# Kernel tuning notes

Hardware: AMD Instinct MI355X
Metric: run time of the kernel (lower is better)

Reference implementation:

```python
import jax, jax.numpy as jnp
import numpy as np

D_MODEL, N_HEADS, D_FF = 768, 12, 3072
B, S = 2, 2048
EPS = 1e-6

def _ln(x, alpha, bias):
    # Matches torch: std with Bessel correction (unbiased), scalar alpha/bias
    mean = x.mean(axis=-1, keepdims=True)
    std = jnp.std(x, axis=-1, keepdims=True, ddof=1)
    return alpha * (x - mean) / (std + EPS) + bias

def setup_inputs() -> dict:
    key = jax.random.key(0)
    ks = jax.random.split(key, 12)
    def w(k, shp):
        return jax.random.normal(k, shp, dtype=jnp.float32) * 0.02
    inp = {
        "x": jax.random.normal(ks[0], (B, S, D_MODEL), dtype=jnp.float32),
        "mask": jnp.ones((B, 1, 1, S), dtype=jnp.int32),
        "wq": w(ks[1], (D_MODEL, D_MODEL)), "bq": jnp.zeros((D_MODEL,), jnp.float32),
        "wk": w(ks[2], (D_MODEL, D_MODEL)), "bk": jnp.zeros((D_MODEL,), jnp.float32),
        "wv": w(ks[3], (D_MODEL, D_MODEL)), "bv": jnp.zeros((D_MODEL,), jnp.float32),
        "wo": w(ks[4], (D_MODEL, D_MODEL)), "bo": jnp.zeros((D_MODEL,), jnp.float32),
        "w1": w(ks[5], (D_MODEL, D_FF)), "b1": jnp.zeros((D_FF,), jnp.float32),
        "w2": w(ks[6], (D_FF, D_MODEL)), "b2": jnp.zeros((D_MODEL,), jnp.float32),
        "ln1_a": jnp.ones((1,), jnp.float32), "ln1_b": jnp.zeros((1,), jnp.float32),
        "ln2_a": jnp.ones((1,), jnp.float32), "ln2_b": jnp.zeros((1,), jnp.float32),
    }
    return inp

def reference(x, mask, wq, bq, wk, bk, wv, bv, wo, bo, w1, b1, w2, b2,
              ln1_a, ln1_b, ln2_a, ln2_b):
    d_k = D_MODEL // N_HEADS
    # --- residual 1: pre-LN self-attention ---
    h = _ln(x, ln1_a, ln1_b)
    q = (h @ wq + bq).reshape(B, S, N_HEADS, d_k).transpose(0, 2, 1, 3)
    k = (h @ wk + bk).reshape(B, S, N_HEADS, d_k).transpose(0, 2, 1, 3)
    v = (h @ wv + bv).reshape(B, S, N_HEADS, d_k).transpose(0, 2, 1, 3)
    scores = jnp.einsum('bhqd,bhkd->bhqk', q, k) / jnp.sqrt(jnp.float32(d_k))
    scores = jnp.where(mask == 0, jnp.float32(-1e9), scores)
    attn = jax.nn.softmax(scores, axis=-1)            # [B,H,S,S] materialized, as in source
    ctx = jnp.einsum('bhqk,bhkd->bhqd', attn, v)
    ctx = ctx.transpose(0, 2, 1, 3).reshape(B, S, D_MODEL)
    x = x + (ctx @ wo + bo)
    # --- residual 2: pre-LN FFN ---
    h = _ln(x, ln2_a, ln2_b)
    ffn = jax.nn.relu(h @ w1 + b1) @ w2 + b2
    return x + ffn
```

## Files before the change

### kernel.cpp

```cpp
#include <hip/hip_runtime.h>
#include <math.h>

#define DM    768
#define NH    12
#define DKH   64
#define DFF   3072
#define BATCH 2
#define SLEN  2048
#define MTOT  4096
#define LNEPS 1e-6f
#define QSCALE 0.18033688011112042f

typedef unsigned short u16;
typedef __attribute__((ext_vector_type(8))) short bf16x8;
typedef __attribute__((ext_vector_type(4))) float f32x4;
typedef __attribute__((ext_vector_type(4))) unsigned short us4;

__device__ __forceinline__ u16 f2bf(float f) {
    union { float f; unsigned int u; } v; v.f = f;
    unsigned int r = v.u + 0x7FFFu + ((v.u >> 16) & 1u);
    return (u16)(r >> 16);
}

__device__ __forceinline__ unsigned pk2bf(float lo, float hi) {
    union { float f; unsigned u; } a, b;
    a.f = lo; b.f = hi;
    return __builtin_amdgcn_perm(b.u + 0x8000u, a.u + 0x8000u, 0x07060302u);
}

__device__ __forceinline__ void gld16(const void* g, void* lds) {
    __builtin_amdgcn_global_load_lds(
        (const __attribute__((address_space(1))) unsigned int*)(unsigned long long)g,
        (__attribute__((address_space(3))) unsigned int*)(unsigned int)(unsigned long long)lds,
        16, 0, 0);
}

__global__ __launch_bounds__(256) void ln_kernel(const float* __restrict__ x,
                                                 u16* __restrict__ out,
                                                 const float* __restrict__ alpha_p,
                                                 const float* __restrict__ beta_p) {
    int row = blockIdx.x;
    const float* xr = x + (size_t)row * DM;
    int t = threadIdx.x;
    float v0 = xr[t], v1 = xr[t + 256], v2 = xr[t + 512];
    float s = v0 + v1 + v2;
    #pragma unroll
    for (int off = 32; off > 0; off >>= 1) s += __shfl_down(s, off);
    __shared__ float red[4], red2[4];
    int wv = t >> 6, ln = t & 63;
    if (ln == 0) red[wv] = s;
    __syncthreads();
    float mean = (red[0] + red[1] + red[2] + red[3]) * (1.0f / 768.0f);
    float d0 = v0 - mean, d1 = v1 - mean, d2 = v2 - mean;
    float sq = d0 * d0 + d1 * d1 + d2 * d2;
    #pragma unroll
    for (int off = 32; off > 0; off >>= 1) sq += __shfl_down(sq, off);
    if (ln == 0) red2[wv] = sq;
    __syncthreads();
    float var = (red2[0] + red2[1] + red2[2] + red2[3]) * (1.0f / 767.0f);
    float scale = alpha_p[0] / (sqrtf(var) + LNEPS);
    float bias = beta_p[0];
    u16* orow = out + (size_t)row * DM;
    orow[t]       = f2bf(d0 * scale + bias);
    orow[t + 256] = f2bf(d1 * scale + bias);
    orow[t + 512] = f2bf(d2 * scale + bias);
}

__global__ __launch_bounds__(256) void wcast_all(
        const float* __restrict__ wq, const float* __restrict__ wk,
        const float* __restrict__ wv, const float* __restrict__ wo,
        const float* __restrict__ w1, const float* __restrict__ w2,
        u16* __restrict__ wqT, u16* __restrict__ wkT, u16* __restrict__ wvT,
        u16* __restrict__ woT, u16* __restrict__ w1T, u16* __restrict__ w2T) {
    __shared__ float tile[32][33];
    int bid = blockIdx.x;
    const float* src; u16* dst; int R, C, bx, by;
    if (bid < 2304) {
        int j = bid / 576, tix = bid % 576;
        R = 768; C = 768; bx = tix % 24; by = tix / 24;
        src = (j == 0) ? wq : (j == 1) ? wk : (j == 2) ? wv : wo;
        dst = (j == 0) ? wqT : (j == 1) ? wkT : (j == 2) ? wvT : woT;
    } else if (bid < 4608) {
        int tix = bid - 2304;
        R = 768; C = 3072; bx = tix % 96; by = tix / 96;
        src = w1; dst = w1T;
    } else {
        int tix = bid - 4608;
        R = 3072; C = 768; bx = tix % 24; by = tix / 24;
        src = w2; dst = w2T;
    }
    int t = threadIdx.x, tx = t & 31, ty = t >> 5;
    int r0 = by * 32, c0 = bx * 32;
    #pragma unroll
    for (int p = 0; p < 4; p++)
        tile[ty + p * 8][tx] = src[(size_t)(r0 + ty + p * 8) * C + c0 + tx];
    __syncthreads();
    #pragma unroll
    for (int p = 0; p < 4; p++)
        dst[(size_t)(c0 + ty + p * 8) * R + r0 + tx] = f2bf(tile[tx][ty + p * 8]);
}

template<int EPI>
__device__ __forceinline__ void gemm128_core(const u16* __restrict__ A,
                                             const u16* __restrict__ Wt,
                                             const float* __restrict__ bias,
                                             const float* __restrict__ resid,
                                             void* __restrict__ Cout,
                                             int M, int N, int Kstride, int Kloop,
                                             float scale, int bm, int bn) {
    __shared__ __align__(16) u16 As[2][128 * 32];
    __shared__ __align__(16) u16 Bs[2][128 * 32];
    int t = threadIdx.x;
    int ln = t & 63, w = t >> 6;
    int wm = w >> 1, wn = w & 1;
    int quad = ln >> 4, col = ln & 15;
    int m0 = bm * 128, n0 = bn * 128;

    f32x4 acc[4][4];
    const f32x4 zero = {0.f, 0.f, 0.f, 0.f};
    #pragma unroll
    for (int i = 0; i < 4; i++)
        #pragma unroll
        for (int j = 0; j < 4; j++) acc[i][j] = zero;

    const u16* Ag = A  + (size_t)(m0 + 32 * w + (ln >> 2)) * Kstride + (ln & 3) * 8;
    const u16* Bg = Wt + (size_t)(n0 + 32 * w + (ln >> 2)) * Kstride + (ln & 3) * 8;

    gld16(Ag,                As[0] + w * 1024);
    gld16(Ag + 16 * Kstride, As[0] + w * 1024 + 512);
    gld16(Bg,                Bs[0] + w * 1024);
    gld16(Bg + 16 * Kstride, Bs[0] + w * 1024 + 512);
    __syncthreads();

    for (int k0 = 0; k0 < Kloop; k0 += 32) {
        int cur = (k0 >> 5) & 1, nxt = cur ^ 1;
        if (k0 + 32 < Kloop) {
            gld16(Ag + k0 + 32,                As[nxt] + w * 1024);
            gld16(Ag + k0 + 32 + 16 * Kstride, As[nxt] + w * 1024 + 512);
            gld16(Bg + k0 + 32,                Bs[nxt] + w * 1024);
            gld16(Bg + k0 + 32 + 16 * Kstride, Bs[nxt] + w * 1024 + 512);
        }
        bf16x8 af[4], bfr[4];
        #pragma unroll
        for (int i = 0; i < 4; i++)
            af[i] = *(const bf16x8*)&As[cur][(wm * 64 + i * 16 + col) * 32 + quad * 8];
        #pragma unroll
        for (int j = 0; j < 4; j++)
            bfr[j] = *(const bf16x8*)&Bs[cur][(wn * 64 + j * 16 + col) * 32 + quad * 8];
        #pragma unroll
        for (int i = 0; i < 4; i++)
            #pragma unroll
            for (int j = 0; j < 4; j++)
                acc[i][j] = __builtin_amdgcn_mfma_f32_16x16x32_bf16(af[i], bfr[j], acc[i][j], 0, 0, 0);
        __syncthreads();
    }

    #pragma unroll
    for (int i = 0; i < 4; i++) {
        int mb = m0 + wm * 64 + i * 16 + quad * 4;
        #pragma unroll
        for (int j = 0; j < 4; j++) {
            int n = n0 + wn * 64 + j * 16 + col;
            if (EPI == 0 || EPI == 1) {
                float bs = bias[n];
                u16* Cb = (u16*)Cout;
                #pragma unroll
                for (int r = 0; r < 4; r++) {
                    float f = (acc[i][j][r] + bs) * ((EPI == 0) ? scale : 1.0f);
                    if (EPI == 1) f = fmaxf(f, 0.f);
                    Cb[(size_t)(mb + r) * N + n] = f2bf(f);
                }
            } else if (EPI == 2) {
                float bs = bias[n];
                float* Cf = (float*)Cout;
                #pragma unroll
                for (int r = 0; r < 4; r++)
                    Cf[(size_t)(mb + r) * N + n] =
                        acc[i][j][r] + bs + resid[(size_t)(mb + r) * N + n];
            } else if (EPI == 3) {
                float bs = bias[n];
                u16* Cb = (u16*)Cout;
                us4 pk;
                #pragma unroll
                for (int r = 0; r < 4; r++) pk[r] = f2bf(acc[i][j][r] + bs);
                *(us4*)&Cb[(size_t)n * M + mb] = pk;
            } else {
                float* Cf = (float*)Cout;
                #pragma unroll
                for (int r = 0; r < 4; r++)
                    atomicAdd(&Cf[(size_t)(mb + r) * N + n], acc[i][j][r]);
            }
        }
    }
}

template<int EPI>
__global__ __launch_bounds__(256) void gemm_kernel(const u16* __restrict__ A,
                                                   const u16* __restrict__ Wt,
                                                   const float* __restrict__ bias,
                                                   const float* __restrict__ resid,
                                                   void* __restrict__ C,
                                                   int M, int N, int Kstride, int Kloop,
                                                   float scale) {
    const u16* Az = A  + (size_t)blockIdx.z * Kloop;
    const u16* Wz = Wt + (size_t)blockIdx.z * Kloop;
    gemm128_core<EPI>(Az, Wz, bias, resid, C, M, N, Kstride, Kloop, scale,
                      blockIdx.y, blockIdx.x);
}

__global__ __launch_bounds__(256) void qkv_kernel(const u16* __restrict__ h,
        const u16* __restrict__ wqT, const u16* __restrict__ wkT, const u16* __restrict__ wvT,
        const float* __restrict__ bq, const float* __restrict__ bk, const float* __restrict__ bv,
        u16* __restrict__ q, u16* __restrict__ k, u16* __restrict__ vT) {
    int z = blockIdx.z;
    if (z == 0)      gemm128_core<0>(h, wqT, bq, nullptr, q,  MTOT, DM, DM, DM, QSCALE, blockIdx.y, blockIdx.x);
    else if (z == 1) gemm128_core<0>(h, wkT, bk, nullptr, k,  MTOT, DM, DM, DM, 1.0f,   blockIdx.y, blockIdx.x);
    else             gemm128_core<3>(h, wvT, bv, nullptr, vT, MTOT, DM, DM, DM, 1.0f,   blockIdx.y, blockIdx.x);
}

template<int EPI>
__global__ __launch_bounds__(256) void gemm64_kernel(const u16* __restrict__ A,
                                                     const u16* __restrict__ Wt,
                                                     const float* __restrict__ bias,
                                                     const float* __restrict__ resid,
                                                     void* __restrict__ Cout,
                                                     int M, int N, int Kstride, int Kloop) {
    __shared__ __align__(16) u16 As[2][64 * 32];
    __shared__ __align__(16) u16 Bs[2][64 * 32];
    int t = threadIdx.x, ln = t & 63, w = t >> 6;
    int wm = w >> 1, wn = w & 1;
    int quad = ln >> 4, col = ln & 15;
    int m0 = blockIdx.y * 64, n0 = blockIdx.x * 64;

    f32x4 acc[2][2];
    const f32x4 zero = {0.f, 0.f, 0.f, 0.f};
    #pragma unroll
    for (int i = 0; i < 2; i++)
        #pragma unroll
        for (int j = 0; j < 2; j++) acc[i][j] = zero;

    const u16* Ag = A  + (size_t)(m0 + 16 * w + (ln >> 2)) * Kstride + (ln & 3) * 8;
    const u16* Bg = Wt + (size_t)(n0 + 16 * w + (ln >> 2)) * Kstride + (ln & 3) * 8;
    gld16(Ag, As[0] + w * 512);
    gld16(Bg, Bs[0] + w * 512);
    __syncthreads();

    for (int k0 = 0; k0 < Kloop; k0 += 32) {
        int cur = (k0 >> 5) & 1, nxt = cur ^ 1;
        if (k0 + 32 < Kloop) {
            gld16(Ag + k0 + 32, As[nxt] + w * 512);
            gld16(Bg + k0 + 32, Bs[nxt] + w * 512);
        }
        bf16x8 af[2], bfr[2];
        #pragma unroll
        for (int i = 0; i < 2; i++)
            af[i] = *(const bf16x8*)&As[cur][(wm * 32 + i * 16 + col) * 32 + quad * 8];
        #pragma unroll
        for (int j = 0; j < 2; j++)
            bfr[j] = *(const bf16x8*)&Bs[cur][(wn * 32 + j * 16 + col) * 32 + quad * 8];
        #pragma unroll
        for (int i = 0; i < 2; i++)
            #pragma unroll
            for (int j = 0; j < 2; j++)
                acc[i][j] = __builtin_amdgcn_mfma_f32_16x16x32_bf16(af[i], bfr[j], acc[i][j], 0, 0, 0);
        __syncthreads();
    }

    #pragma unroll
    for (int i = 0; i < 2; i++) {
        int mb = m0 + wm * 32 + i * 16 + quad * 4;
        #pragma unroll
        for (int j = 0; j < 2; j++) {
            int n = n0 + wn * 32 + j * 16 + col;
            float bs = bias[n];
            float* Cf = (float*)Cout;
            #pragma unroll
            for (int r = 0; r < 4; r++)
                Cf[(size_t)(mb + r) * N + n] =
                    acc[i][j][r] + bs + resid[(size_t)(mb + r) * N + n];
        }
    }
}

__global__ __launch_bounds__(256) void init_out(const float* __restrict__ x1,
                                                const float* __restrict__ b2,
                                                float* __restrict__ out) {
    int e = (blockIdx.x * 256 + threadIdx.x) * 4;
    float4 xv = *(const float4*)&x1[e];
    float4 bv = *(const float4*)&b2[e % DM];
    float4 o;
    o.x = xv.x + bv.x; o.y = xv.y + bv.y; o.z = xv.z + bv.z; o.w = xv.w + bv.w;
    *(float4*)&out[e] = o;
}

__global__ __launch_bounds__(256) void attn_kernel(const u16* __restrict__ qg,
                                                   const u16* __restrict__ kg,
                                                   const u16* __restrict__ vTg,
                                                   const int* __restrict__ mask,
                                                   u16* __restrict__ ctx) {
    __shared__ __align__(16) u16 Qs[64 * 64];
    __shared__ __align__(16) u16 Ks[2][64 * 64];
    __shared__ __align__(16) u16 Vt[2][64 * 64];
    __shared__ __align__(16) u16 Ps[4][16 * 72];
    __shared__ int Ms[2][64];
    int t = threadIdx.x, ln = t & 63, w = t >> 6;
    int quad = ln >> 4, col = ln & 15;
    int bh = blockIdx.x, qb = blockIdx.y;
    int b = bh / NH, h = bh - b * NH;
    int q0 = qb * 64;
    size_t qkbase = ((size_t)b * SLEN) * DM + h * DKH;
    size_t vbase  = ((size_t)h * DKH) * MTOT + (size_t)b * SLEN;

    int sw_st = (((ln & 7) ^ (ln >> 3)) * 8);
    int c0 = ((quad ^ (ln & 7)) * 8);
    int c1 = c0 ^ 32;

    {
        const u16* g0 = qg + qkbase + (size_t)(q0 + 16 * w + (ln >> 3)) * DM + sw_st;
        gld16(g0,          Qs + w * 1024);
        gld16(g0 + 8 * DM, Qs + w * 1024 + 512);
        const u16* kg0 = kg + qkbase + (size_t)(16 * w + (ln >> 3)) * DM + sw_st;
        gld16(kg0,          Ks[0] + w * 1024);
        gld16(kg0 + 8 * DM, Ks[0] + w * 1024 + 512);
        const u16* vg0 = vTg + vbase + (size_t)(16 * w + (ln >> 3)) * MTOT + sw_st;
        gld16(vg0,            Vt[0] + w * 1024);
        gld16(vg0 + 8 * MTOT, Vt[0] + w * 1024 + 512);
        if (t < 64) Ms[0][t] = mask[b * SLEN + t];
    }
    __syncthreads();

    int rowQ = (w * 16 + col) * 64;
    bf16x8 bq0 = *(const bf16x8*)&Qs[rowQ + c0];
    bf16x8 bq1 = *(const bf16x8*)&Qs[rowQ + c1];

    const u16* kpn = kg + qkbase + (size_t)(64 + 16 * w + (ln >> 3)) * DM + sw_st;
    const u16* vpn = vTg + vbase + (size_t)(16 * w + (ln >> 3)) * MTOT + 64 + sw_st;
    const int* mpn = mask + b * SLEN + 64 + t;

    float lacc = 0.f;
    f32x4 Ov[4];
    const f32x4 zero = {0.f, 0.f, 0.f, 0.f};
    #pragma unroll
    for (int j = 0; j < 4; j++) Ov[j] = zero;
    u16* Psw = &Ps[w][0];

    for (int j0 = 0; j0 < SLEN; j0 += 64) {
        int cur = (j0 >> 6) & 1, nxt = cur ^ 1;
        if (j0 + 64 < SLEN) {
            gld16(kpn,          Ks[nxt] + w * 1024);
            gld16(kpn + 8 * DM, Ks[nxt] + w * 1024 + 512);
            gld16(vpn,            Vt[nxt] + w * 1024);
            gld16(vpn + 8 * MTOT, Vt[nxt] + w * 1024 + 512);
            if (t < 64) Ms[nxt][t] = *mpn;
            kpn += 64 * DM; vpn += 64; mpn += 64;
        }

        f32x4 S[4];
        #pragma unroll
        for (int j = 0; j < 4; j++) {
            int rk = (j * 16 + col) * 64;
            bf16x8 ak0 = *(const bf16x8*)&Ks[cur][rk + c0];
            bf16x8 ak1 = *(const bf16x8*)&Ks[cur][rk + c1];
            f32x4 s = __builtin_amdgcn_mfma_f32_16x16x32_bf16(ak0, bq0, zero, 0, 0, 0);
            S[j]     = __builtin_amdgcn_mfma_f32_16x16x32_bf16(ak1, bq1, s,    0, 0, 0);
        }
        #pragma unroll
        for (int j = 0; j < 4; j++) {
            int m4[4];
            *(int4*)m4 = *(const int4*)&Ms[cur][j * 16 + quad * 4];
            float p0 = exp2f((m4[0] == 0) ? -1e9f : S[j][0]);
            float p1 = exp2f((m4[1] == 0) ? -1e9f : S[j][1]);
            float p2 = exp2f((m4[2] == 0) ? -1e9f : S[j][2]);
            float p3 = exp2f((m4[3] == 0) ? -1e9f : S[j][3]);
            lacc += (p0 + p1) + (p2 + p3);
            uint2 pk;
            pk.x = pk2bf(p0, p1);
            pk.y = pk2bf(p2, p3);
            *(uint2*)&Psw[col * 72 + j * 16 + quad * 4] = pk;
        }
        bf16x8 ap0 = *(const bf16x8*)&Psw[col * 72 + quad * 8];
        bf16x8 ap1 = *(const bf16x8*)&Psw[col * 72 + 32 + quad * 8];
        #pragma unroll
        for (int j = 0; j < 4; j++) {
            int rv = (j * 16 + col) * 64;
            bf16x8 bv0 = *(const bf16x8*)&Vt[cur][rv + c0];
            bf16x8 bv1 = *(const bf16x8*)&Vt[cur][rv + c1];
            Ov[j] = __builtin_amdgcn_mfma_f32_16x16x32_bf16(ap0, bv0, Ov[j], 0, 0, 0);
            Ov[j] = __builtin_amdgcn_mfma_f32_16x16x32_bf16(ap1, bv1, Ov[j], 0, 0, 0);
        }
        __syncthreads();
    }
    lacc += __shfl_xor(lacc, 16);
    lacc += __shfl_xor(lacc, 32);
    float linv = 1.0f / lacc;
    float invr[4];
    #pragma unroll
    for (int r = 0; r < 4; r++) invr[r] = __shfl(linv, quad * 4 + r);
    #pragma unroll
    for (int j = 0; j < 4; j++)
        #pragma unroll
        for (int r = 0; r < 4; r++)
            ctx[qkbase + (size_t)(q0 + w * 16 + quad * 4 + r) * DM + j * 16 + col] =
                f2bf(Ov[j][r] * invr[r]);
}

extern "C" void kernel_launch(void* const* d_in, const int* in_sizes, int n_in,
                              void* d_out, int out_size, void* d_ws, size_t ws_size,
                              hipStream_t stream) {
    const float* x    = (const float*)d_in[0];
    const int*   mask = (const int*)d_in[1];
    const float* wq   = (const float*)d_in[2];
    const float* bq   = (const float*)d_in[3];
    const float* wk   = (const float*)d_in[4];
    const float* bk   = (const float*)d_in[5];
    const float* wv   = (const float*)d_in[6];
    const float* bv   = (const float*)d_in[7];
    const float* wo   = (const float*)d_in[8];
    const float* bo   = (const float*)d_in[9];
    const float* w1   = (const float*)d_in[10];
    const float* b1   = (const float*)d_in[11];
    const float* w2   = (const float*)d_in[12];
    const float* b2   = (const float*)d_in[13];
    const float* ln1a = (const float*)d_in[14];
    const float* ln1b = (const float*)d_in[15];
    const float* ln2a = (const float*)d_in[16];
    const float* ln2b = (const float*)d_in[17];
    float* out = (float*)d_out;

    char* w8 = (char*)d_ws;
    u16*   ffn = (u16*)(w8 + 0);
    u16*   q   = (u16*)(w8 + 0);
    u16*   kb  = (u16*)(w8 + 6291456);
    u16*   vT  = (u16*)(w8 + 12582912);
    u16*   ctx = (u16*)(w8 + 18874368);
    u16*   h   = (u16*)(w8 + 25165824);
    float* x1  = (float*)(w8 + 31457280);
    u16*   wqT = (u16*)(w8 + 44040192);
    u16*   wkT = (u16*)(w8 + 45219840);
    u16*   wvT = (u16*)(w8 + 46399488);
    u16*   woT = (u16*)(w8 + 47579136);
    u16*   w1T = (u16*)(w8 + 48758784);
    u16*   w2T = (u16*)(w8 + 53477376);

    wcast_all<<<6912, 256, 0, stream>>>(wq, wk, wv, wo, w1, w2,
                                        wqT, wkT, wvT, woT, w1T, w2T);
    ln_kernel<<<MTOT, 256, 0, stream>>>(x, h, ln1a, ln1b);
    qkv_kernel<<<dim3(6, 32, 3), 256, 0, stream>>>(h, wqT, wkT, wvT, bq, bk, bv, q, kb, vT);
    attn_kernel<<<dim3(BATCH * NH, SLEN / 64), 256, 0, stream>>>(q, kb, vT, mask, ctx);
    gemm64_kernel<2><<<dim3(12, 64), 256, 0, stream>>>(ctx, woT, bo, x, (void*)x1,
                                                       MTOT, DM, DM, DM);
    ln_kernel<<<MTOT, 256, 0, stream>>>(x1, h, ln2a, ln2b);
    gemm_kernel<1><<<dim3(24, 32), 256, 0, stream>>>(h, w1T, b1, nullptr, (void*)ffn,
                                                     MTOT, DFF, DM, DM, 1.0f);
    init_out<<<MTOT * DM / 1024, 256, 0, stream>>>(x1, b2, out);
    gemm_kernel<5><<<dim3(6, 32, 2), 256, 0, stream>>>(ffn, w2T, nullptr, nullptr, (void*)out,
                                                       MTOT, DM, DFF, DFF / 2, 1.0f);
}
```

Before: 310.5 us.

## Split attention waves over query and key halves, fuse init_out into layernorm

The attention kernel now has each wave handle 32 queries by 32 keys instead of 16 queries by 64 keys. This lets K and V fragments be reused across two query groups and combines the two key halves through LDS at the end. The mask is folded into the MFMA accumulator as a precomputed additive bias. Rounding is dropped from the P-to-bf16 pack, so values truncate instead of rounding. Separately, the residual-plus-b2 initialization of the output is folded into the second layernorm kernel, which removes one launch and one re-read of x1, at the cost of an LDS reduction and an extra barrier in attention.

After: 295.1 us. 5.0% less time.

```diff
diff --git a/kernel.cpp b/kernel.cpp
--- a/kernel.cpp
+++ b/kernel.cpp
@@ -22,10 +22,10 @@
     return (u16)(r >> 16);
 }
 
-__device__ __forceinline__ unsigned pk2bf(float lo, float hi) {
+__device__ __forceinline__ unsigned pk2bf_t(float lo, float hi) {
     union { float f; unsigned u; } a, b;
     a.f = lo; b.f = hi;
-    return __builtin_amdgcn_perm(b.u + 0x8000u, a.u + 0x8000u, 0x07060302u);
+    return __builtin_amdgcn_perm(b.u, a.u, 0x07060302u);
 }
 
 __device__ __forceinline__ void gld16(const void* g, void* lds) {
@@ -38,7 +38,9 @@
 __global__ __launch_bounds__(256) void ln_kernel(const float* __restrict__ x,
                                                  u16* __restrict__ out,
                                                  const float* __restrict__ alpha_p,
-                                                 const float* __restrict__ beta_p) {
+                                                 const float* __restrict__ beta_p,
+                                                 const float* __restrict__ b2,
+                                                 float* __restrict__ out2) {
     int row = blockIdx.x;
     const float* xr = x + (size_t)row * DM;
     int t = threadIdx.x;
@@ -64,6 +66,12 @@
     orow[t]       = f2bf(d0 * scale + bias);
     orow[t + 256] = f2bf(d1 * scale + bias);
     orow[t + 512] = f2bf(d2 * scale + bias);
+    if (out2) {
+        float* o2 = out2 + (size_t)row * DM;
+        o2[t]       = v0 + b2[t];
+        o2[t + 256] = v1 + b2[t + 256];
+        o2[t + 512] = v2 + b2[t + 512];
+    }
 }
 
 __global__ __launch_bounds__(256) void wcast_all(
@@ -282,29 +290,19 @@
     }
 }
 
-__global__ __launch_bounds__(256) void init_out(const float* __restrict__ x1,
-                                                const float* __restrict__ b2,
-                                                float* __restrict__ out) {
-    int e = (blockIdx.x * 256 + threadIdx.x) * 4;
-    float4 xv = *(const float4*)&x1[e];
-    float4 bv = *(const float4*)&b2[e % DM];
-    float4 o;
-    o.x = xv.x + bv.x; o.y = xv.y + bv.y; o.z = xv.z + bv.z; o.w = xv.w + bv.w;
-    *(float4*)&out[e] = o;
-}
-
 __global__ __launch_bounds__(256) void attn_kernel(const u16* __restrict__ qg,
                                                    const u16* __restrict__ kg,
                                                    const u16* __restrict__ vTg,
                                                    const int* __restrict__ mask,
                                                    u16* __restrict__ ctx) {
     __shared__ __align__(16) u16 Qs[64 * 64];
-    __shared__ __align__(16) u16 Ks[2][64 * 64];
-    __shared__ __align__(16) u16 Vt[2][64 * 64];
-    __shared__ __align__(16) u16 Ps[4][16 * 72];
-    __shared__ int Ms[2][64];
+    __shared__ __align__(16) u16 KV[4][64 * 64];
+    __shared__ __align__(16) u16 Ps[4][32 * 40];
+    __shared__ __align__(16) float Msf[2][64];
+    __shared__ float Lp[64][2];
     int t = threadIdx.x, ln = t & 63, w = t >> 6;
     int quad = ln >> 4, col = ln & 15;
+    int qh = w >> 1, kh = w & 1;
     int bh = blockIdx.x, qb = blockIdx.y;
     int b = bh / NH, h = bh - b * NH;
     int q0 = qb * 64;
@@ -312,96 +310,129 @@
     size_t vbase  = ((size_t)h * DKH) * MTOT + (size_t)b * SLEN;
 
     int sw_st = (((ln & 7) ^ (ln >> 3)) * 8);
-    int c0 = ((quad ^ (ln & 7)) * 8);
-    int c1 = c0 ^ 32;
 
     {
         const u16* g0 = qg + qkbase + (size_t)(q0 + 16 * w + (ln >> 3)) * DM + sw_st;
         gld16(g0,          Qs + w * 1024);
         gld16(g0 + 8 * DM, Qs + w * 1024 + 512);
         const u16* kg0 = kg + qkbase + (size_t)(16 * w + (ln >> 3)) * DM + sw_st;
-        gld16(kg0,          Ks[0] + w * 1024);
-        gld16(kg0 + 8 * DM, Ks[0] + w * 1024 + 512);
+        gld16(kg0,          KV[0] + w * 1024);
+        gld16(kg0 + 8 * DM, KV[0] + w * 1024 + 512);
         const u16* vg0 = vTg + vbase + (size_t)(16 * w + (ln >> 3)) * MTOT + sw_st;
-        gld16(vg0,            Vt[0] + w * 1024);
-        gld16(vg0 + 8 * MTOT, Vt[0] + w * 1024 + 512);
-        if (t < 64) Ms[0][t] = mask[b * SLEN + t];
-    }
-    __syncthreads();
-
-    int rowQ = (w * 16 + col) * 64;
-    bf16x8 bq0 = *(const bf16x8*)&Qs[rowQ + c0];
-    bf16x8 bq1 = *(const bf16x8*)&Qs[rowQ + c1];
+        gld16(vg0,            KV[2] + w * 1024);
+        gld16(vg0 + 8 * MTOT, KV[2] + w * 1024 + 512);
+        if (t < 64) Msf[0][t] = mask[b * SLEN + t] ? 0.f : -1e9f;
+    }
+    __syncthreads();
+
+    bf16x8 bqf[2][2];
+    #pragma unroll
+    for (int qgi = 0; qgi < 2; qgi++) {
+        int rq = qh * 32 + qgi * 16 + col;
+        int cq = ((quad ^ (rq & 7)) * 8);
+        bqf[qgi][0] = *(const bf16x8*)&Qs[rq * 64 + cq];
+        bqf[qgi][1] = *(const bf16x8*)&Qs[rq * 64 + (cq ^ 32)];
+    }
 
     const u16* kpn = kg + qkbase + (size_t)(64 + 16 * w + (ln >> 3)) * DM + sw_st;
     const u16* vpn = vTg + vbase + (size_t)(16 * w + (ln >> 3)) * MTOT + 64 + sw_st;
     const int* mpn = mask + b * SLEN + 64 + t;
 
-    float lacc = 0.f;
-    f32x4 Ov[4];
+    float lacc[2] = {0.f, 0.f};
+    f32x4 Ov[2][4];
     const f32x4 zero = {0.f, 0.f, 0.f, 0.f};
     #pragma unroll
-    for (int j = 0; j < 4; j++) Ov[j] = zero;
+    for (int qgi = 0; qgi < 2; qgi++)
+        #pragma unroll
+        for (int dg = 0; dg < 4; dg++) Ov[qgi][dg] = zero;
     u16* Psw = &Ps[w][0];
 
     for (int j0 = 0; j0 < SLEN; j0 += 64) {
         int cur = (j0 >> 6) & 1, nxt = cur ^ 1;
         if (j0 + 64 < SLEN) {
-            gld16(kpn,          Ks[nxt] + w * 1024);
-            gld16(kpn + 8 * DM, Ks[nxt] + w * 1024 + 512);
-            gld16(vpn,            Vt[nxt] + w * 1024);
-            gld16(vpn + 8 * MTOT, Vt[nxt] + w * 1024 + 512);
-            if (t < 64) Ms[nxt][t] = *mpn;
+            gld16(kpn,            KV[nxt] + w * 1024);
+            gld16(kpn + 8 * DM,   KV[nxt] + w * 1024 + 512);
+            gld16(vpn,            KV[2 + nxt] + w * 1024);
+            gld16(vpn + 8 * MTOT, KV[2 + nxt] + w * 1024 + 512);
+            if (t < 64) Msf[nxt][t] = *mpn ? 0.f : -1e9f;
             kpn += 64 * DM; vpn += 64; mpn += 64;
         }
 
-        f32x4 S[4];
-        #pragma unroll
-        for (int j = 0; j < 4; j++) {
-            int rk = (j * 16 + col) * 64;
-            bf16x8 ak0 = *(const bf16x8*)&Ks[cur][rk + c0];
-            bf16x8 ak1 = *(const bf16x8*)&Ks[cur][rk + c1];
-            f32x4 s = __builtin_amdgcn_mfma_f32_16x16x32_bf16(ak0, bq0, zero, 0, 0, 0);
-            S[j]     = __builtin_amdgcn_mfma_f32_16x16x32_bf16(ak1, bq1, s,    0, 0, 0);
-        }
-        #pragma unroll
-        for (int j = 0; j < 4; j++) {
-            int m4[4];
-            *(int4*)m4 = *(const int4*)&Ms[cur][j * 16 + quad * 4];
-            float p0 = exp2f((m4[0] == 0) ? -1e9f : S[j][0]);
-            float p1 = exp2f((m4[1] == 0) ? -1e9f : S[j][1]);
-            float p2 = exp2f((m4[2] == 0) ? -1e9f : S[j][2]);
-            float p3 = exp2f((m4[3] == 0) ? -1e9f : S[j][3]);
-            lacc += (p0 + p1) + (p2 + p3);
-            uint2 pk;
-            pk.x = pk2bf(p0, p1);
-            pk.y = pk2bf(p2, p3);
-            *(uint2*)&Psw[col * 72 + j * 16 + quad * 4] = pk;
-        }
-        bf16x8 ap0 = *(const bf16x8*)&Psw[col * 72 + quad * 8];
-        bf16x8 ap1 = *(const bf16x8*)&Psw[col * 72 + 32 + quad * 8];
-        #pragma unroll
-        for (int j = 0; j < 4; j++) {
-            int rv = (j * 16 + col) * 64;
-            bf16x8 bv0 = *(const bf16x8*)&Vt[cur][rv + c0];
-            bf16x8 bv1 = *(const bf16x8*)&Vt[cur][rv + c1];
-            Ov[j] = __builtin_amdgcn_mfma_f32_16x16x32_bf16(ap0, bv0, Ov[j], 0, 0, 0);
-            Ov[j] = __builtin_amdgcn_mfma_f32_16x16x32_bf16(ap1, bv1, Ov[j], 0, 0, 0);
+        bf16x8 ak[2][2];
+        #pragma unroll
+        for (int kgi = 0; kgi < 2; kgi++) {
+            int rk = kh * 32 + kgi * 16 + col;
+            int ck = ((quad ^ (rk & 7)) * 8);
+            ak[kgi][0] = *(const bf16x8*)&KV[cur][rk * 64 + ck];
+            ak[kgi][1] = *(const bf16x8*)&KV[cur][rk * 64 + (ck ^ 32)];
+        }
+        #pragma unroll
+        for (int kgi = 0; kgi < 2; kgi++) {
+            f32x4 bias4 = *(const f32x4*)&Msf[cur][kh * 32 + kgi * 16 + quad * 4];
+            #pragma unroll
+            for (int qgi = 0; qgi < 2; qgi++) {
+                f32x4 S = __builtin_amdgcn_mfma_f32_16x16x32_bf16(ak[kgi][0], bqf[qgi][0], bias4, 0, 0, 0);
+                S       = __builtin_amdgcn_mfma_f32_16x16x32_bf16(ak[kgi][1], bqf[qgi][1], S,     0, 0, 0);
+                float p0 = exp2f(S[0]), p1 = exp2f(S[1]);
+                float p2 = exp2f(S[2]), p3 = exp2f(S[3]);
+                lacc[qgi] += (p0 + p1) + (p2 + p3);
+                uint2 pk;
+                pk.x = pk2bf_t(p0, p1);
+                pk.y = pk2bf_t(p2, p3);
+                *(uint2*)&Psw[(qgi * 16 + col) * 40 + kgi * 16 + quad * 4] = pk;
+            }
+        }
+        bf16x8 ap[2];
+        #pragma unroll
+        for (int qgi = 0; qgi < 2; qgi++)
+            ap[qgi] = *(const bf16x8*)&Psw[(qgi * 16 + col) * 40 + quad * 8];
+        #pragma unroll
+        for (int dg = 0; dg < 4; dg++) {
+            int rv = dg * 16 + col;
+            int cv = (((kh * 4 + quad) ^ (rv & 7)) * 8);
+            bf16x8 bv = *(const bf16x8*)&KV[2 + cur][rv * 64 + cv];
+            Ov[0][dg] = __builtin_amdgcn_mfma_f32_16x16x32_bf16(ap[0], bv, Ov[0][dg], 0, 0, 0);
+            Ov[1][dg] = __builtin_amdgcn_mfma_f32_16x16x32_bf16(ap[1], bv, Ov[1][dg], 0, 0, 0);
         }
         __syncthreads();
     }
-    lacc += __shfl_xor(lacc, 16);
-    lacc += __shfl_xor(lacc, 32);
-    float linv = 1.0f / lacc;
-    float invr[4];
-    #pragma unroll
-    for (int r = 0; r < 4; r++) invr[r] = __shfl(linv, quad * 4 + r);
-    #pragma unroll
-    for (int j = 0; j < 4; j++)
-        #pragma unroll
-        for (int r = 0; r < 4; r++)
-            ctx[qkbase + (size_t)(q0 + w * 16 + quad * 4 + r) * DM + j * 16 + col] =
-                f2bf(Ov[j][r] * invr[r]);
+
+    #pragma unroll
+    for (int qgi = 0; qgi < 2; qgi++) {
+        lacc[qgi] += __shfl_xor(lacc[qgi], 16);
+        lacc[qgi] += __shfl_xor(lacc[qgi], 32);
+        if (quad == 0) Lp[qh * 32 + qgi * 16 + col][kh] = lacc[qgi];
+    }
+    float* Osh = (float*)&KV[0][0];
+    if (kh == 1) {
+        #pragma unroll
+        for (int qgi = 0; qgi < 2; qgi++)
+            #pragma unroll
+            for (int dg = 0; dg < 4; dg++)
+                *(f32x4*)&Osh[(qh * 64 + dg * 16 + col) * 36 + qgi * 16 + quad * 4] = Ov[qgi][dg];
+    }
+    __syncthreads();
+    if (kh == 0) {
+        #pragma unroll
+        for (int qgi = 0; qgi < 2; qgi++) {
+            float linv[4];
+            #pragma unroll
+            for (int r = 0; r < 4; r++) {
+                int ql = qh * 32 + qgi * 16 + quad * 4 + r;
+                linv[r] = 1.0f / (Lp[ql][0] + Lp[ql][1]);
+            }
+            #pragma unroll
+            for (int dg = 0; dg < 4; dg++) {
+                f32x4 oo = *(const f32x4*)&Osh[(qh * 64 + dg * 16 + col) * 36 + qgi * 16 + quad * 4];
+                #pragma unroll
+                for (int r = 0; r < 4; r++) {
+                    int qrow = q0 + qh * 32 + qgi * 16 + quad * 4 + r;
+                    ctx[qkbase + (size_t)qrow * DM + dg * 16 + col] =
+                        f2bf((Ov[qgi][dg][r] + oo[r]) * linv[r]);
+                }
+            }
+        }
+    }
 }
 
 extern "C" void kernel_launch(void* const* d_in, const int* in_sizes, int n_in,
@@ -444,15 +475,14 @@
 
     wcast_all<<<6912, 256, 0, stream>>>(wq, wk, wv, wo, w1, w2,
                                         wqT, wkT, wvT, woT, w1T, w2T);
-    ln_kernel<<<MTOT, 256, 0, stream>>>(x, h, ln1a, ln1b);
+    ln_kernel<<<MTOT, 256, 0, stream>>>(x, h, ln1a, ln1b, nullptr, nullptr);
     qkv_kernel<<<dim3(6, 32, 3), 256, 0, stream>>>(h, wqT, wkT, wvT, bq, bk, bv, q, kb, vT);
     attn_kernel<<<dim3(BATCH * NH, SLEN / 64), 256, 0, stream>>>(q, kb, vT, mask, ctx);
     gemm64_kernel<2><<<dim3(12, 64), 256, 0, stream>>>(ctx, woT, bo, x, (void*)x1,
                                                        MTOT, DM, DM, DM);
-    ln_kernel<<<MTOT, 256, 0, stream>>>(x1, h, ln2a, ln2b);
+    ln_kernel<<<MTOT, 256, 0, stream>>>(x1, h, ln2a, ln2b, b2, out);
     gemm_kernel<1><<<dim3(24, 32), 256, 0, stream>>>(h, w1T, b1, nullptr, (void*)ffn,
                                                      MTOT, DFF, DM, DM, 1.0f);
-    init_out<<<MTOT * DM / 1024, 256, 0, stream>>>(x1, b2, out);
     gemm_kernel<5><<<dim3(6, 32, 2), 256, 0, stream>>>(ffn, w2T, nullptr, nullptr, (void*)out,
                                                        MTOT, DM, DFF, DFF / 2, 1.0f);
 }
```
